# Optimization experiments

Measured on AMD Instinct MI355X. Metric: run time of the kernel, lower is better.

Reference implementation:

```python
import jax, jax.numpy as jnp
import numpy as np

THRESHOLD = 1.0
NEG_SLOPE = 0.2
N_NODES = 100000
N_EDGES = 1600000
DIM = 64
N_LAYERS = 3


def setup_inputs() -> dict:
    key = jax.random.key(0)
    ks = jax.random.split(key, 6)
    x = jax.random.normal(ks[0], (N_NODES, DIM), dtype=jnp.float32)
    edge_index = jax.random.randint(ks[1], (2, N_EDGES), 0, N_NODES, dtype=jnp.int64)
    scale = 1.0 / np.sqrt(DIM)
    W = jax.random.normal(ks[2], (N_LAYERS, DIM, DIM), dtype=jnp.float32) * scale
    a_src = jax.random.normal(ks[3], (N_LAYERS, DIM), dtype=jnp.float32) * scale
    a_dst = jax.random.normal(ks[4], (N_LAYERS, DIM), dtype=jnp.float32) * scale
    b = jnp.zeros((N_LAYERS, DIM), dtype=jnp.float32)
    return {"x": x, "edge_index": edge_index, "W": W, "a_src": a_src, "a_dst": a_dst, "b": b}


def reference(x, edge_index, W, a_src, a_dst, b):
    N = x.shape[0]
    # GATConv default add_self_loops=True: append (i -> i) for every node
    self_loop = jnp.arange(N, dtype=edge_index.dtype)
    src = jnp.concatenate([edge_index[0], self_loop])  # message source j
    dst = jnp.concatenate([edge_index[1], self_loop])  # message target i

    h = x
    for l in range(W.shape[0]):
        hw = h @ W[l]                       # [N, d] linear transform
        alpha_s = hw @ a_src[l]             # [N] per-node src attention logits
        alpha_d = hw @ a_dst[l]             # [N] per-node dst attention logits
        e = jax.nn.leaky_relu(alpha_s[src] + alpha_d[dst], NEG_SLOPE)  # [E']
        # softmax over incoming edges of each dst node (segment softmax)
        m = jax.ops.segment_max(e, dst, num_segments=N)
        p = jnp.exp(e - m[dst])
        s = jax.ops.segment_sum(p, dst, num_segments=N)
        attn = p / s[dst]
        out = jax.ops.segment_sum(attn[:, None] * hw[src], dst, num_segments=N)
        h = jnp.clip(out + b[l], -THRESHOLD, THRESHOLD)  # act_fn = clamp
    return h
```

## Files before the change

kernel.cpp:

```cpp
#include <hip/hip_runtime.h>
#include <hip/hip_fp16.h>

#define NN 100000
#define NE 1600000
#define DIM 64
#define NL 3
#define SLOPE 0.2f

#define BSH 9
#define NBUCK ((NN + 511) >> BSH)
#define EPT 16
#define TILE (256 * EPT)
#define MT 128

static __device__ __forceinline__ float lrelu(float x) { return x > 0.f ? x : SLOPE * x; }

static __device__ __forceinline__ float4 load_h4(const ushort* __restrict__ base, size_t off) {
    uint2 u = *(const uint2*)(base + off);
    __half2 h0 = __builtin_bit_cast(__half2, u.x);
    __half2 h1 = __builtin_bit_cast(__half2, u.y);
    float2 f0 = __half22float2(h0);
    float2 f1 = __half22float2(h1);
    return make_float4(f0.x, f0.y, f1.x, f1.y);
}


__global__ __launch_bounds__(256) void k_bucket_hist(const int* __restrict__ ei, int* __restrict__ bcnt) {
    __shared__ int h[256];
    int t = threadIdx.x;
    h[t] = 0;
    __syncthreads();
    const int4* d4 = (const int4*)(ei + NE);
    int idx = blockIdx.x * 256 + t;
    if (idx < NE / 4) {
        int4 v = d4[idx];
        atomicAdd(&h[v.x >> BSH], 1);
        atomicAdd(&h[v.y >> BSH], 1);
        atomicAdd(&h[v.z >> BSH], 1);
        atomicAdd(&h[v.w >> BSH], 1);
    }
    __syncthreads();
    if (t < NBUCK && h[t]) atomicAdd(&bcnt[t], h[t]);
}

__global__ void k_bucket_scan(const int* __restrict__ bcnt, int* __restrict__ bbase, int* __restrict__ bcur,
                              int* __restrict__ offs) {
    __shared__ int sm[256];
    int t = threadIdx.x;
    sm[t] = (t < NBUCK) ? bcnt[t] : 0;
    __syncthreads();
    for (int off = 1; off < 256; off <<= 1) {
        int x = (t >= off) ? sm[t - off] : 0;
        __syncthreads();
        sm[t] += x;
        __syncthreads();
    }
    if (t < NBUCK) {
        int ex = (t == 0) ? 0 : sm[t - 1];
        bbase[t] = ex;
        bcur[t] = ex;
    }
    if (t == 0) {
        bbase[NBUCK] = NE;
        offs[NN] = NE;
    }
}

__global__ __launch_bounds__(256) void k_partition(const int* __restrict__ ei, int* __restrict__ bcur,
                                                   int2* __restrict__ pairs) {
    __shared__ int2 tile[TILE];
    __shared__ int cnt[256], ofsx[256], gdel[256], sm[256];
    int t = threadIdx.x;
    int ts = blockIdx.x * TILE;
    int tilecnt = NE - ts;
    if (tilecnt > TILE) tilecnt = TILE;
    cnt[t] = 0;
    __syncthreads();
    int srcv[EPT], dstv[EPT], rk[EPT];
    int ebase = ts + t * EPT;
    if (ts + TILE <= NE) {
#pragma unroll
        for (int j = 0; j < EPT / 4; j++) {
            int4 sv = *(const int4*)(ei + ebase + j * 4);
            int4 dv = *(const int4*)(ei + NE + ebase + j * 4);
            srcv[j * 4 + 0] = sv.x;
            srcv[j * 4 + 1] = sv.y;
            srcv[j * 4 + 2] = sv.z;
            srcv[j * 4 + 3] = sv.w;
            dstv[j * 4 + 0] = dv.x;
            dstv[j * 4 + 1] = dv.y;
            dstv[j * 4 + 2] = dv.z;
            dstv[j * 4 + 3] = dv.w;
        }
#pragma unroll
        for (int k = 0; k < EPT; k++) rk[k] = atomicAdd(&cnt[dstv[k] >> BSH], 1);
    } else {
#pragma unroll
        for (int k = 0; k < EPT; k++) {
            int e = ebase + k;
            if (e < NE) {
                srcv[k] = ei[e];
                dstv[k] = ei[NE + e];
                rk[k] = atomicAdd(&cnt[dstv[k] >> BSH], 1);
            } else {
                rk[k] = -1;
            }
        }
    }
    __syncthreads();
    sm[t] = cnt[t];
    __syncthreads();
    for (int off = 1; off < 256; off <<= 1) {
        int x = (t >= off) ? sm[t - off] : 0;
        __syncthreads();
        sm[t] += x;
        __syncthreads();
    }
    ofsx[t] = (t == 0) ? 0 : sm[t - 1];
    __syncthreads();
    if (ts + TILE <= NE) {
#pragma unroll
        for (int k = 0; k < EPT; k++) tile[ofsx[dstv[k] >> BSH] + rk[k]] = make_int2(srcv[k], dstv[k]);
    } else {
#pragma unroll
        for (int k = 0; k < EPT; k++)
            if (rk[k] >= 0) tile[ofsx[dstv[k] >> BSH] + rk[k]] = make_int2(srcv[k], dstv[k]);
    }
    if (t < NBUCK && cnt[t]) gdel[t] = atomicAdd(&bcur[t], cnt[t]) - ofsx[t];
    __syncthreads();
    for (int i = t; i < tilecnt; i += 256) {
        int2 p = tile[i];
        pairs[gdel[p.y >> BSH] + i] = p;
    }
}

__global__ __launch_bounds__(256) void k_node_csr(const int2* __restrict__ pairs, const int* __restrict__ bbase,
                                                  int* __restrict__ offs, int* __restrict__ csr) {
    __shared__ int deg[512], sofs[512], scur[512], sm[256];
    int t = threadIdx.x;
    int b = blockIdx.x;
    int nodeBase = b << BSH;
    int nNodes = NN - nodeBase;
    if (nNodes > 512) nNodes = 512;
    deg[t] = 0;
    deg[t + 256] = 0;
    __syncthreads();
    int ebeg = bbase[b], eend = bbase[b + 1];
    for (int i = ebeg + t; i < eend; i += 256) atomicAdd(&deg[pairs[i].y - nodeBase], 1);
    __syncthreads();
    int a0 = deg[2 * t], a1 = deg[2 * t + 1];
    sm[t] = a0 + a1;
    __syncthreads();
    for (int off = 1; off < 256; off <<= 1) {
        int x = (t >= off) ? sm[t - off] : 0;
        __syncthreads();
        sm[t] += x;
        __syncthreads();
    }
    int base = (t == 0) ? 0 : sm[t - 1];
    sofs[2 * t] = base;
    sofs[2 * t + 1] = base + a0;
    scur[2 * t] = 0;
    scur[2 * t + 1] = 0;
    __syncthreads();
    for (int n = t; n < nNodes; n += 256) offs[nodeBase + n] = ebeg + sofs[n];
    for (int i = ebeg + t; i < eend; i += 256) {
        int2 p = pairs[i];
        int ln = p.y - nodeBase;
        int r = atomicAdd(&scur[ln], 1);
        csr[ebeg + sofs[ln] + r] = p.x;
    }
}


__global__ __launch_bounds__(256) void k_transform(const float* __restrict__ h, const float* __restrict__ W,
                                                   const float* __restrict__ avs, const float* __restrict__ avd,
                                                   ushort* __restrict__ hw, float* __restrict__ als,
                                                   float* __restrict__ ald) {
    __shared__ float sh[MT][65];
    __shared__ float sw[64][64];
    int t = threadIdx.x;
    int tx = t & 15, ty = t >> 4;
    int base = blockIdx.x * MT;
    int rows = NN - base;
    if (rows > MT) rows = MT;
    {
        const float4* Wv = (const float4*)W;
        float4* swv = (float4*)sw;
        for (int i = t; i < 1024; i += 256) swv[i] = Wv[i];
    }
    for (int i = t; i < MT * 16; i += 256) {
        int r = i >> 4, cs = i & 15;
        float4 v = (r < rows) ? *(const float4*)(h + (size_t)(base + r) * 64 + cs * 4)
                              : make_float4(0.f, 0.f, 0.f, 0.f);
        sh[r][cs * 4 + 0] = v.x;
        sh[r][cs * 4 + 1] = v.y;
        sh[r][cs * 4 + 2] = v.z;
        sh[r][cs * 4 + 3] = v.w;
    }
    __syncthreads();
    float acc[8][4] = {};
    int r0 = ty * 8;
#pragma unroll 4
    for (int k = 0; k < 64; k++) {
        float4 b = *(const float4*)(&sw[k][tx * 4]);
#pragma unroll
        for (int r = 0; r < 8; r++) {
            float a = sh[r0 + r][k];
            acc[r][0] = fmaf(a, b.x, acc[r][0]);
            acc[r][1] = fmaf(a, b.y, acc[r][1]);
            acc[r][2] = fmaf(a, b.z, acc[r][2]);
            acc[r][3] = fmaf(a, b.w, acc[r][3]);
        }
    }
    float4 as4 = *(const float4*)(avs + tx * 4);
    float4 ad4 = *(const float4*)(avd + tx * 4);
#pragma unroll
    for (int r = 0; r < 8; r++) {
        int row = r0 + r;
        bool ok = row < rows;
        if (ok) {
            __half2 h0 = __floats2half2_rn(acc[r][0], acc[r][1]);
            __half2 h1 = __floats2half2_rn(acc[r][2], acc[r][3]);
            uint2 u;
            u.x = __builtin_bit_cast(unsigned int, h0);
            u.y = __builtin_bit_cast(unsigned int, h1);
            *(uint2*)(hw + (size_t)(base + row) * 64 + tx * 4) = u;
        }
        float ps = acc[r][0] * as4.x + acc[r][1] * as4.y + acc[r][2] * as4.z + acc[r][3] * as4.w;
        float pd = acc[r][0] * ad4.x + acc[r][1] * ad4.y + acc[r][2] * ad4.z + acc[r][3] * ad4.w;
#pragma unroll
        for (int off = 1; off <= 8; off <<= 1) {
            ps += __shfl_xor(ps, off);
            pd += __shfl_xor(pd, off);
        }
        if (tx == 0 && ok) {
            als[base + row] = ps;
            ald[base + row] = pd;
        }
    }
}

__global__ __launch_bounds__(256) void k_aggregate(const ushort* __restrict__ hw, const float* __restrict__ als,
                                                   const float* __restrict__ ald, const int* __restrict__ offs,
                                                   const int* __restrict__ csr, const float* __restrict__ bv,
                                                   float* __restrict__ out) {
    int t = threadIdx.x, wave = t >> 6, lane = t & 63;
    int grp = lane >> 4, l = lane & 15;
    int grpbase = grp << 4;
    int i = blockIdx.x * 16 + wave * 4 + grp;
    if (i >= NN) return;
    float ad = ald[i];
    float spart = 0.f;
    float4 acc = make_float4(0.f, 0.f, 0.f, 0.f);
    int beg = offs[i], end = offs[i + 1];
    for (int cb = beg; cb < end; cb += 16) {
        int cnt = end - cb;
        if (cnt > 16) cnt = 16;
        int src = 0;
        float p = 0.f;
        if (l < cnt) {
            src = csr[cb + l];
            p = __expf(lrelu(als[src] + ad));
        }
        spart += p;
        int iters = (cnt + 3) >> 2;
        for (int j = 0; j < iters; j++) {
            int jb = grpbase + j * 4;
            int s0 = __shfl(src, jb);
            int s1 = __shfl(src, jb + 1);
            int s2 = __shfl(src, jb + 2);
            int s3 = __shfl(src, jb + 3);
            float p0 = __shfl(p, jb);
            float p1 = __shfl(p, jb + 1);
            float p2 = __shfl(p, jb + 2);
            float p3 = __shfl(p, jb + 3);
            float4 v0 = load_h4(hw, (size_t)s0 * 64 + l * 4);
            float4 v1 = load_h4(hw, (size_t)s1 * 64 + l * 4);
            float4 v2 = load_h4(hw, (size_t)s2 * 64 + l * 4);
            float4 v3 = load_h4(hw, (size_t)s3 * 64 + l * 4);
            acc.x = fmaf(p0, v0.x, acc.x);
            acc.y = fmaf(p0, v0.y, acc.y);
            acc.z = fmaf(p0, v0.z, acc.z);
            acc.w = fmaf(p0, v0.w, acc.w);
            acc.x = fmaf(p1, v1.x, acc.x);
            acc.y = fmaf(p1, v1.y, acc.y);
            acc.z = fmaf(p1, v1.z, acc.z);
            acc.w = fmaf(p1, v1.w, acc.w);
            acc.x = fmaf(p2, v2.x, acc.x);
            acc.y = fmaf(p2, v2.y, acc.y);
            acc.z = fmaf(p2, v2.z, acc.z);
            acc.w = fmaf(p2, v2.w, acc.w);
            acc.x = fmaf(p3, v3.x, acc.x);
            acc.y = fmaf(p3, v3.y, acc.y);
            acc.z = fmaf(p3, v3.z, acc.z);
            acc.w = fmaf(p3, v3.w, acc.w);
        }
    }
    float s = spart;
#pragma unroll
    for (int off = 1; off <= 8; off <<= 1) s += __shfl_xor(s, off);
    float ps = __expf(lrelu(als[i] + ad));
    s += ps;
    float4 hv = load_h4(hw, (size_t)i * 64 + l * 4);
    acc.x = fmaf(ps, hv.x, acc.x);
    acc.y = fmaf(ps, hv.y, acc.y);
    acc.z = fmaf(ps, hv.z, acc.z);
    acc.w = fmaf(ps, hv.w, acc.w);
    float inv = 1.f / s;
    const float4 bq = *(const float4*)(bv + l * 4);
    float4 o;
    o.x = fminf(fmaxf(fmaf(acc.x, inv, bq.x), -1.f), 1.f);
    o.y = fminf(fmaxf(fmaf(acc.y, inv, bq.y), -1.f), 1.f);
    o.z = fminf(fmaxf(fmaf(acc.z, inv, bq.z), -1.f), 1.f);
    o.w = fminf(fmaxf(fmaf(acc.w, inv, bq.w), -1.f), 1.f);
    *(float4*)(out + (size_t)i * 64 + l * 4) = o;
}


extern "C" void kernel_launch(void* const* d_in, const int* in_sizes, int n_in, void* d_out, int out_size,
                              void* d_ws, size_t ws_size, hipStream_t stream) {
    const float* x = (const float*)d_in[0];
    const int* ei = (const int*)d_in[1];
    const float* W = (const float*)d_in[2];
    const float* a_s = (const float*)d_in[3];
    const float* a_d = (const float*)d_in[4];
    const float* b = (const float*)d_in[5];
    float* out = (float*)d_out;

    char* w = (char*)d_ws;
    auto alloc = [&](size_t bytes) -> char* {
        char* p = w;
        w += (bytes + 255) & ~(size_t)255;
        return p;
    };
    int* bcnt = (int*)alloc(256 * 4);
    int* bbase = (int*)alloc(257 * 4);
    int* bcur = (int*)alloc(256 * 4);
    int* offs = (int*)alloc((NN + 1) * 4);
    int* csr = (int*)alloc((size_t)NE * 4);
    size_t layer_bytes = (size_t)(2 * NN) * 4 + (size_t)NN * DIM * 2;
    size_t build_bytes = (size_t)NE * 8;
    char* region = alloc(layer_bytes > build_bytes ? layer_bytes : build_bytes);
    int2* pairs = (int2*)region;
    float* als = (float*)region;
    float* ald = als + NN;
    ushort* hwb = (ushort*)(ald + NN);

    hipMemsetAsync(bcnt, 0, 256 * 4, stream);
    k_bucket_hist<<<(NE / 4 + 255) / 256, 256, 0, stream>>>(ei, bcnt);
    k_bucket_scan<<<1, 256, 0, stream>>>(bcnt, bbase, bcur, offs);
    k_partition<<<(NE + TILE - 1) / TILE, 256, 0, stream>>>(ei, bcur, pairs);
    k_node_csr<<<NBUCK, 256, 0, stream>>>(pairs, bbase, offs, csr);

    const float* hin = x;
    for (int l = 0; l < NL; l++) {
        k_transform<<<(NN + MT - 1) / MT, 256, 0, stream>>>(hin, W + l * DIM * DIM, a_s + l * DIM, a_d + l * DIM,
                                                            hwb, als, ald);
        k_aggregate<<<(NN + 15) / 16, 256, 0, stream>>>(hwb, als, ald, offs, csr, b + l * DIM, out);
        hin = out;
    }
}
```

Measured before the change: 336.0 us.

## Sort nodes by degree for aggregation and gather 16-byte half-precision rows

The CSR build kernel now records a per-node degree histogram. Two small new kernels turn that histogram into a degree-sorted node permutation, which the aggregate kernel walks so that groups within a wave handle nodes with similar edge counts and diverge less. The gather is also restructured: each 16-lane group splits into two halves that take alternating edges, loading 8 fp16 values (16 bytes) per lane, and the halves are merged with one xor-shuffle at the end. The cost is extra setup kernels and atomics, output writes and offset reads that are no longer sequential, and half the lanes sitting idle during the final store.

```diff
diff --git a/kernel.cpp b/kernel.cpp
--- a/kernel.cpp
+++ b/kernel.cpp
@@ -14,15 +14,6 @@
 #define MT 128
 
 static __device__ __forceinline__ float lrelu(float x) { return x > 0.f ? x : SLOPE * x; }
-
-static __device__ __forceinline__ float4 load_h4(const ushort* __restrict__ base, size_t off) {
-    uint2 u = *(const uint2*)(base + off);
-    __half2 h0 = __builtin_bit_cast(__half2, u.x);
-    __half2 h1 = __builtin_bit_cast(__half2, u.y);
-    float2 f0 = __half22float2(h0);
-    float2 f1 = __half22float2(h1);
-    return make_float4(f0.x, f0.y, f1.x, f1.y);
-}
 
 
 __global__ __launch_bounds__(256) void k_bucket_hist(const int* __restrict__ ei, int* __restrict__ bcnt) {
@@ -135,8 +126,9 @@
 }
 
 __global__ __launch_bounds__(256) void k_node_csr(const int2* __restrict__ pairs, const int* __restrict__ bbase,
-                                                  int* __restrict__ offs, int* __restrict__ csr) {
-    __shared__ int deg[512], sofs[512], scur[512], sm[256];
+                                                  int* __restrict__ offs, int* __restrict__ csr,
+                                                  int* __restrict__ dcnt) {
+    __shared__ int deg[512], sofs[512], scur[512], sm[256], dh[64];
     int t = threadIdx.x;
     int b = blockIdx.x;
     int nodeBase = b << BSH;
@@ -144,6 +136,7 @@
     if (nNodes > 512) nNodes = 512;
     deg[t] = 0;
     deg[t + 256] = 0;
+    if (t < 64) dh[t] = 0;
     __syncthreads();
     int ebeg = bbase[b], eend = bbase[b + 1];
     for (int i = ebeg + t; i < eend; i += 256) atomicAdd(&deg[pairs[i].y - nodeBase], 1);
@@ -163,12 +156,43 @@
     scur[2 * t] = 0;
     scur[2 * t + 1] = 0;
     __syncthreads();
-    for (int n = t; n < nNodes; n += 256) offs[nodeBase + n] = ebeg + sofs[n];
+    for (int n = t; n < nNodes; n += 256) {
+        offs[nodeBase + n] = ebeg + sofs[n];
+        int d = deg[n];
+        atomicAdd(&dh[d > 63 ? 63 : d], 1);
+    }
     for (int i = ebeg + t; i < eend; i += 256) {
         int2 p = pairs[i];
         int ln = p.y - nodeBase;
         int r = atomicAdd(&scur[ln], 1);
         csr[ebeg + sofs[ln] + r] = p.x;
+    }
+    __syncthreads();
+    if (t < 64 && dh[t]) atomicAdd(&dcnt[t], dh[t]);
+}
+
+__global__ void k_degscan(const int* __restrict__ dcnt, int* __restrict__ dcur) {
+    __shared__ int sm[64];
+    int t = threadIdx.x;
+    sm[t] = dcnt[t];
+    __syncthreads();
+    for (int off = 1; off < 64; off <<= 1) {
+        int x = (t >= off) ? sm[t - off] : 0;
+        __syncthreads();
+        sm[t] += x;
+        __syncthreads();
+    }
+    dcur[t] = (t == 0) ? 0 : sm[t - 1];
+}
+
+__global__ __launch_bounds__(256) void k_degscatter(const int* __restrict__ offs, int* __restrict__ dcur,
+                                                    int* __restrict__ nodeperm) {
+    int i = blockIdx.x * 256 + threadIdx.x;
+    if (i < NN) {
+        int d = offs[i + 1] - offs[i];
+        if (d > 63) d = 63;
+        int pos = atomicAdd(&dcur[d], 1);
+        nodeperm[pos] = i;
     }
 }
 
@@ -243,16 +267,19 @@
 
 __global__ __launch_bounds__(256) void k_aggregate(const ushort* __restrict__ hw, const float* __restrict__ als,
                                                    const float* __restrict__ ald, const int* __restrict__ offs,
-                                                   const int* __restrict__ csr, const float* __restrict__ bv,
-                                                   float* __restrict__ out) {
+                                                   const int* __restrict__ csr, const int* __restrict__ nodeperm,
+                                                   const float* __restrict__ bv, float* __restrict__ out) {
     int t = threadIdx.x, wave = t >> 6, lane = t & 63;
     int grp = lane >> 4, l = lane & 15;
     int grpbase = grp << 4;
-    int i = blockIdx.x * 16 + wave * 4 + grp;
-    if (i >= NN) return;
+    int gid = blockIdx.x * 16 + wave * 4 + grp;
+    if (gid >= NN) return;
+    int i = nodeperm[gid];
+    int halfsel = l >> 3;
+    int dimoff = (l & 7) * 8;
     float ad = ald[i];
     float spart = 0.f;
-    float4 acc = make_float4(0.f, 0.f, 0.f, 0.f);
+    float acc[8] = {};
     int beg = offs[i], end = offs[i + 1];
     for (int cb = beg; cb < end; cb += 16) {
         int cnt = end - cb;
@@ -264,57 +291,78 @@
             p = __expf(lrelu(als[src] + ad));
         }
         spart += p;
-        int iters = (cnt + 3) >> 2;
-        for (int j = 0; j < iters; j++) {
-            int jb = grpbase + j * 4;
-            int s0 = __shfl(src, jb);
-            int s1 = __shfl(src, jb + 1);
-            int s2 = __shfl(src, jb + 2);
-            int s3 = __shfl(src, jb + 3);
-            float p0 = __shfl(p, jb);
-            float p1 = __shfl(p, jb + 1);
-            float p2 = __shfl(p, jb + 2);
-            float p3 = __shfl(p, jb + 3);
-            float4 v0 = load_h4(hw, (size_t)s0 * 64 + l * 4);
-            float4 v1 = load_h4(hw, (size_t)s1 * 64 + l * 4);
-            float4 v2 = load_h4(hw, (size_t)s2 * 64 + l * 4);
-            float4 v3 = load_h4(hw, (size_t)s3 * 64 + l * 4);
-            acc.x = fmaf(p0, v0.x, acc.x);
-            acc.y = fmaf(p0, v0.y, acc.y);
-            acc.z = fmaf(p0, v0.z, acc.z);
-            acc.w = fmaf(p0, v0.w, acc.w);
-            acc.x = fmaf(p1, v1.x, acc.x);
-            acc.y = fmaf(p1, v1.y, acc.y);
-            acc.z = fmaf(p1, v1.z, acc.z);
-            acc.w = fmaf(p1, v1.w, acc.w);
-            acc.x = fmaf(p2, v2.x, acc.x);
-            acc.y = fmaf(p2, v2.y, acc.y);
-            acc.z = fmaf(p2, v2.z, acc.z);
-            acc.w = fmaf(p2, v2.w, acc.w);
-            acc.x = fmaf(p3, v3.x, acc.x);
-            acc.y = fmaf(p3, v3.y, acc.y);
-            acc.z = fmaf(p3, v3.z, acc.z);
-            acc.w = fmaf(p3, v3.w, acc.w);
-        }
-    }
+        int pairs2 = (cnt + 1) >> 1;
+        for (int j = 0; j < pairs2; j += 2) {
+            int ea = grpbase + j * 2 + halfsel;
+            int eb = ea + 2;
+            int sa = __shfl(src, ea);
+            float pa = __shfl(p, ea);
+            int sb = __shfl(src, eb);
+            float pb = __shfl(p, eb);
+            uint4 ua = *(const uint4*)(hw + (size_t)sa * 64 + dimoff);
+            uint4 ub = *(const uint4*)(hw + (size_t)sb * 64 + dimoff);
+            float2 f0 = __half22float2(__builtin_bit_cast(__half2, ua.x));
+            float2 f1 = __half22float2(__builtin_bit_cast(__half2, ua.y));
+            float2 f2 = __half22float2(__builtin_bit_cast(__half2, ua.z));
+            float2 f3 = __half22float2(__builtin_bit_cast(__half2, ua.w));
+            acc[0] = fmaf(pa, f0.x, acc[0]);
+            acc[1] = fmaf(pa, f0.y, acc[1]);
+            acc[2] = fmaf(pa, f1.x, acc[2]);
+            acc[3] = fmaf(pa, f1.y, acc[3]);
+            acc[4] = fmaf(pa, f2.x, acc[4]);
+            acc[5] = fmaf(pa, f2.y, acc[5]);
+            acc[6] = fmaf(pa, f3.x, acc[6]);
+            acc[7] = fmaf(pa, f3.y, acc[7]);
+            float2 g0 = __half22float2(__builtin_bit_cast(__half2, ub.x));
+            float2 g1 = __half22float2(__builtin_bit_cast(__half2, ub.y));
+            float2 g2 = __half22float2(__builtin_bit_cast(__half2, ub.z));
+            float2 g3 = __half22float2(__builtin_bit_cast(__half2, ub.w));
+            acc[0] = fmaf(pb, g0.x, acc[0]);
+            acc[1] = fmaf(pb, g0.y, acc[1]);
+            acc[2] = fmaf(pb, g1.x, acc[2]);
+            acc[3] = fmaf(pb, g1.y, acc[3]);
+            acc[4] = fmaf(pb, g2.x, acc[4]);
+            acc[5] = fmaf(pb, g2.y, acc[5]);
+            acc[6] = fmaf(pb, g3.x, acc[6]);
+            acc[7] = fmaf(pb, g3.y, acc[7]);
+        }
+    }
+#pragma unroll
+    for (int k = 0; k < 8; k++) acc[k] += __shfl_xor(acc[k], 8);
     float s = spart;
 #pragma unroll
     for (int off = 1; off <= 8; off <<= 1) s += __shfl_xor(s, off);
     float ps = __expf(lrelu(als[i] + ad));
     s += ps;
-    float4 hv = load_h4(hw, (size_t)i * 64 + l * 4);
-    acc.x = fmaf(ps, hv.x, acc.x);
-    acc.y = fmaf(ps, hv.y, acc.y);
-    acc.z = fmaf(ps, hv.z, acc.z);
-    acc.w = fmaf(ps, hv.w, acc.w);
-    float inv = 1.f / s;
-    const float4 bq = *(const float4*)(bv + l * 4);
-    float4 o;
-    o.x = fminf(fmaxf(fmaf(acc.x, inv, bq.x), -1.f), 1.f);
-    o.y = fminf(fmaxf(fmaf(acc.y, inv, bq.y), -1.f), 1.f);
-    o.z = fminf(fmaxf(fmaf(acc.z, inv, bq.z), -1.f), 1.f);
-    o.w = fminf(fmaxf(fmaf(acc.w, inv, bq.w), -1.f), 1.f);
-    *(float4*)(out + (size_t)i * 64 + l * 4) = o;
+    uint4 uh = *(const uint4*)(hw + (size_t)i * 64 + dimoff);
+    float2 h0 = __half22float2(__builtin_bit_cast(__half2, uh.x));
+    float2 h1 = __half22float2(__builtin_bit_cast(__half2, uh.y));
+    float2 h2 = __half22float2(__builtin_bit_cast(__half2, uh.z));
+    float2 h3 = __half22float2(__builtin_bit_cast(__half2, uh.w));
+    acc[0] = fmaf(ps, h0.x, acc[0]);
+    acc[1] = fmaf(ps, h0.y, acc[1]);
+    acc[2] = fmaf(ps, h1.x, acc[2]);
+    acc[3] = fmaf(ps, h1.y, acc[3]);
+    acc[4] = fmaf(ps, h2.x, acc[4]);
+    acc[5] = fmaf(ps, h2.y, acc[5]);
+    acc[6] = fmaf(ps, h3.x, acc[6]);
+    acc[7] = fmaf(ps, h3.y, acc[7]);
+    if (halfsel == 0) {
+        float inv = 1.f / s;
+        const float4 b0 = *(const float4*)(bv + dimoff);
+        const float4 b1 = *(const float4*)(bv + dimoff + 4);
+        float4 o0, o1;
+        o0.x = fminf(fmaxf(fmaf(acc[0], inv, b0.x), -1.f), 1.f);
+        o0.y = fminf(fmaxf(fmaf(acc[1], inv, b0.y), -1.f), 1.f);
+        o0.z = fminf(fmaxf(fmaf(acc[2], inv, b0.z), -1.f), 1.f);
+        o0.w = fminf(fmaxf(fmaf(acc[3], inv, b0.w), -1.f), 1.f);
+        o1.x = fminf(fmaxf(fmaf(acc[4], inv, b1.x), -1.f), 1.f);
+        o1.y = fminf(fmaxf(fmaf(acc[5], inv, b1.y), -1.f), 1.f);
+        o1.z = fminf(fmaxf(fmaf(acc[6], inv, b1.z), -1.f), 1.f);
+        o1.w = fminf(fmaxf(fmaf(acc[7], inv, b1.w), -1.f), 1.f);
+        *(float4*)(out + (size_t)i * 64 + dimoff) = o0;
+        *(float4*)(out + (size_t)i * 64 + dimoff + 4) = o1;
+    }
 }
 
 
@@ -334,10 +382,13 @@
         w += (bytes + 255) & ~(size_t)255;
         return p;
     };
-    int* bcnt = (int*)alloc(256 * 4);
+    int* bcnt = (int*)alloc((256 + 64) * 4);
+    int* dcnt = bcnt + 256;
     int* bbase = (int*)alloc(257 * 4);
     int* bcur = (int*)alloc(256 * 4);
+    int* dcur = (int*)alloc(64 * 4);
     int* offs = (int*)alloc((NN + 1) * 4);
+    int* nodeperm = (int*)alloc(NN * 4);
     int* csr = (int*)alloc((size_t)NE * 4);
     size_t layer_bytes = (size_t)(2 * NN) * 4 + (size_t)NN * DIM * 2;
     size_t build_bytes = (size_t)NE * 8;
@@ -347,17 +398,19 @@
     float* ald = als + NN;
     ushort* hwb = (ushort*)(ald + NN);
 
-    hipMemsetAsync(bcnt, 0, 256 * 4, stream);
+    hipMemsetAsync(bcnt, 0, (256 + 64) * 4, stream);
     k_bucket_hist<<<(NE / 4 + 255) / 256, 256, 0, stream>>>(ei, bcnt);
     k_bucket_scan<<<1, 256, 0, stream>>>(bcnt, bbase, bcur, offs);
     k_partition<<<(NE + TILE - 1) / TILE, 256, 0, stream>>>(ei, bcur, pairs);
-    k_node_csr<<<NBUCK, 256, 0, stream>>>(pairs, bbase, offs, csr);
+    k_node_csr<<<NBUCK, 256, 0, stream>>>(pairs, bbase, offs, csr, dcnt);
+    k_degscan<<<1, 64, 0, stream>>>(dcnt, dcur);
+    k_degscatter<<<(NN + 255) / 256, 256, 0, stream>>>(offs, dcur, nodeperm);
 
     const float* hin = x;
     for (int l = 0; l < NL; l++) {
         k_transform<<<(NN + MT - 1) / MT, 256, 0, stream>>>(hin, W + l * DIM * DIM, a_s + l * DIM, a_d + l * DIM,
                                                             hwb, als, ald);
-        k_aggregate<<<(NN + 15) / 16, 256, 0, stream>>>(hwb, als, ald, offs, csr, b + l * DIM, out);
+        k_aggregate<<<(NN + 15) / 16, 256, 0, stream>>>(hwb, als, ald, offs, csr, nodeperm, b + l * DIM, out);
         hin = out;
     }
 }
```

New measurement: 606.6 us. 80.5% more time.
